# Performance work log

Hardware: AMD Instinct MI355X
Metric: run time of the kernel (lower is better)

The kernel has to match this reference:

```python
import jax, jax.numpy as jnp
import numpy as np

IN_OCT = 512
OUT_OCT = 512
BATCH = 512


def setup_inputs() -> dict:
    key = jax.random.key(0)
    kx, kw = jax.random.split(key)
    x = jax.random.normal(kx, (BATCH, IN_OCT * 8), dtype=jnp.float32)
    weight = jax.random.normal(kw, (OUT_OCT, IN_OCT, 8, 8), dtype=jnp.float32)
    bias = jnp.zeros((OUT_OCT, 8), dtype=jnp.float32)
    return {"x": x, "weight": weight, "bias": bias}


def reference(x, weight, bias):
    # x: [B, in_oct*8]; weight: [out_oct, in_oct, 8, 8]; bias: [out_oct, 8]
    B = x.shape[0]
    out_oct, in_oct = weight.shape[0], weight.shape[1]
    xo = x.reshape(B, in_oct, 8)
    # octonion_mul(x[:, j], weight[i, j]) applies the per-pair 8x8 octonion
    # left-multiplication matrix; summed over j it is one bilinear contraction.
    y = jnp.einsum("bjp,ijpk->bik", xo, weight) + bias[None, :, :]
    return y.reshape(B, out_oct * 8)
```

## Files before the change

kernel.cpp:

```cpp
#include <hip/hip_runtime.h>
#include <stdint.h>


#define M_DIM 512
#define N_DIM 4096
#define K_DIM 4096
#define KSPLIT 4
#define KC (K_DIM / KSPLIT)
#define NIT (KC / 32)
#define PART_ELEMS (M_DIM * N_DIM)

typedef __bf16 bf16x8 __attribute__((ext_vector_type(8)));
typedef float f32x4 __attribute__((ext_vector_type(4)));

__device__ inline unsigned short f2bf(float f) {
  union { float f; unsigned int u; } v;
  v.f = f;
  unsigned int u = v.u;
  unsigned int r = (u + 0x7fffu + ((u >> 16) & 1u)) >> 16;
  return (unsigned short)r;
}

__global__ __launch_bounds__(256) void prep_kernel(
    const float* __restrict__ x, const float* __restrict__ w,
    const float* __restrict__ bias, unsigned short* __restrict__ abf,
    unsigned short* __restrict__ bt, float* __restrict__ out) {
  const int bid = blockIdx.x;
  const int t = threadIdx.x;
  if (bid < 4096) {
    __shared__ __align__(16) unsigned short lT[8][512];
    const int i = bid >> 3;
    const int jg = bid & 7;
    const float4* src =
        (const float4*)(w + (size_t)i * 32768 + jg * 4096 + t * 16);
    float4 v0 = src[0], v1 = src[1], v2 = src[2], v3 = src[3];
    const int jp = (t >> 2) * 8 + (t & 3) * 2;
    const float* lo = (const float*)&v0;
    const float* hi = (const float*)&v2;
#pragma unroll
    for (int k = 0; k < 4; ++k) {
      unsigned int pk =
          (unsigned int)f2bf(lo[k]) | ((unsigned int)f2bf(hi[k]) << 16);
      *(unsigned int*)&lT[k][jp] = pk;
    }
    lo = (const float*)&v1;
    hi = (const float*)&v3;
#pragma unroll
    for (int k = 0; k < 4; ++k) {
      unsigned int pk =
          (unsigned int)f2bf(lo[k]) | ((unsigned int)f2bf(hi[k]) << 16);
      *(unsigned int*)&lT[k + 4][jp] = pk;
    }
    __syncthreads();
    const int r = t >> 5, c = t & 31;
    const uint4* s = (const uint4*)&lT[r][c * 16];
    uint4* d = (uint4*)(bt + (size_t)(i * 8 + r) * K_DIM + jg * 512 + c * 16);
    d[0] = s[0];
    d[1] = s[1];
  } else if (bid < 5120) {
    int g = (bid - 4096) * 256 + t;
    const float4* xi = (const float4*)x;
    float4 a = xi[g * 2];
    float4 b = xi[g * 2 + 1];
    __attribute__((aligned(16))) unsigned short o[8] = {
        f2bf(a.x), f2bf(a.y), f2bf(a.z), f2bf(a.w),
        f2bf(b.x), f2bf(b.y), f2bf(b.z), f2bf(b.w)};
    *(uint4*)(abf + (size_t)g * 8) = *(const uint4*)o;
  } else {
    int g = (bid - 5120) * 256 + t;
    int el = g * 4;
    int col = el & (N_DIM - 1);
    *(float4*)(out + el) = *(const float4*)(bias + col);
  }
}

__device__ inline void gld16(const void* g, void* l) {
  __builtin_amdgcn_global_load_lds(
      (const __attribute__((address_space(1))) unsigned int*)g,
      (__attribute__((address_space(3))) unsigned int*)l, 16, 0, 0);
}

__global__ __launch_bounds__(256) void gemm_kernel(
    const unsigned short* __restrict__ A, const unsigned short* __restrict__ Bt,
    float* __restrict__ out, float* __restrict__ part, int use_atomic) {
  __shared__ __align__(16) char lds[2][16 * 1024];
  const int t = threadIdx.x;
  const int n0 = blockIdx.x * 128;
  const int m0 = blockIdx.y * 128;
  const int z = blockIdx.z;
  const int kc0 = z * KC;
  const int w = t >> 6;
  const int lane = t & 63;
  const int wr = w >> 1;
  const int wc = w & 1;
  const int lrow = lane & 15;
  const int kb = lane >> 4;
  const int kslot = (kb + (lrow >> 1)) & 3;

  f32x4 acc[4][4] = {};

  const int srow = t >> 2;
  const int gslot = ((t & 3) - ((t >> 3) & 3)) & 3;
  const int scol = gslot * 8;
  const size_t aOff0 = (size_t)(m0 + srow) * K_DIM + kc0 + scol;
  const size_t aOff1 = aOff0 + (size_t)64 * K_DIM;
  const size_t bOff0 = (size_t)(n0 + srow) * K_DIM + kc0 + scol;
  const size_t bOff1 = bOff0 + (size_t)64 * K_DIM;

  auto issue = [&](int it) {
    char* buf = lds[it & 1];
    gld16(A + aOff0 + it * 32, buf + t * 16);
    gld16(A + aOff1 + it * 32, buf + 4096 + t * 16);
    gld16(Bt + bOff0 + it * 32, buf + 8192 + t * 16);
    gld16(Bt + bOff1 + it * 32, buf + 12288 + t * 16);
  };

  issue(0);
  for (int it = 0; it < NIT; ++it) {
    __syncthreads();
    if (it + 1 < NIT) issue(it + 1);
    const unsigned short* cA = (const unsigned short*)lds[it & 1];
    const unsigned short* cB = cA + 4096;

    bf16x8 af[4], bfr[4];
#pragma unroll
    for (int mt = 0; mt < 4; ++mt)
      af[mt] =
          *(const bf16x8*)(cA + (wr * 64 + mt * 16 + lrow) * 32 + kslot * 8);
#pragma unroll
    for (int nt = 0; nt < 4; ++nt)
      bfr[nt] =
          *(const bf16x8*)(cB + (wc * 64 + nt * 16 + lrow) * 32 + kslot * 8);
#pragma unroll
    for (int mt = 0; mt < 4; ++mt)
#pragma unroll
      for (int nt = 0; nt < 4; ++nt)
        acc[mt][nt] = __builtin_amdgcn_mfma_f32_16x16x32_bf16(
            af[mt], bfr[nt], acc[mt][nt], 0, 0, 0);
  }

#pragma unroll
  for (int mt = 0; mt < 4; ++mt) {
    const int gmb = m0 + wr * 64 + mt * 16 + kb * 4;
#pragma unroll
    for (int nt = 0; nt < 4; ++nt) {
      const int gn = n0 + wc * 64 + nt * 16 + lrow;
      if (use_atomic) {
#pragma unroll
        for (int r = 0; r < 4; ++r)
          atomicAdd(out + (size_t)(gmb + r) * N_DIM + gn, acc[mt][nt][r]);
      } else {
        float* p = part + (size_t)z * PART_ELEMS;
#pragma unroll
        for (int r = 0; r < 4; ++r)
          p[(size_t)(gmb + r) * N_DIM + gn] = acc[mt][nt][r];
      }
    }
  }
}

__global__ __launch_bounds__(256) void reduce_kernel(
    const float* __restrict__ part, const float* __restrict__ bias,
    float* __restrict__ out) {
  const int g = blockIdx.x * 256 + threadIdx.x;
  const float4* p = (const float4*)part;
  const float4* b4 = (const float4*)bias;
  const int Q = PART_ELEMS / 4;
  float4 s0 = p[g];
  float4 s1 = p[g + Q];
  float4 s2 = p[g + 2 * Q];
  float4 s3 = p[g + 3 * Q];
  float4 bb = b4[g & (N_DIM / 4 - 1)];
  float4 r;
  r.x = s0.x + s1.x + s2.x + s3.x + bb.x;
  r.y = s0.y + s1.y + s2.y + s3.y + bb.y;
  r.z = s0.z + s1.z + s2.z + s3.z + bb.z;
  r.w = s0.w + s1.w + s2.w + s3.w + bb.w;
  ((float4*)out)[g] = r;
}

extern "C" void kernel_launch(void* const* d_in, const int* in_sizes, int n_in,
                              void* d_out, int out_size, void* d_ws,
                              size_t ws_size, hipStream_t stream) {
  const float* x = (const float*)d_in[0];
  const float* w = (const float*)d_in[1];
  const float* bias = (const float*)d_in[2];
  float* out = (float*)d_out;

  unsigned short* abf = (unsigned short*)d_ws;
  unsigned short* bt = abf + (size_t)M_DIM * K_DIM;
  float* part = (float*)((char*)d_ws + 36u * 1024 * 1024);

  const bool have_ws = ws_size >= 68ull * 1024 * 1024;
  const int use_atomic = have_ws ? 0 : 1;

  prep_kernel<<<use_atomic ? 7168 : 5120, 256, 0, stream>>>(x, w, bias, abf,
                                                            bt, out);

  dim3 grid(N_DIM / 128, M_DIM / 128, KSPLIT);
  gemm_kernel<<<grid, 256, 0, stream>>>(abf, bt, out, part, use_atomic);

  if (!use_atomic)
    reduce_kernel<<<PART_ELEMS / 4 / 256, 256, 0, stream>>>(part, bias, out);
}
```

Before: 138.1 us.

## Fuse fp32-to-bf16 conversion and weight transpose into GEMM tile loads

```diff
diff --git a/kernel.cpp b/kernel.cpp
--- a/kernel.cpp
+++ b/kernel.cpp
@@ -13,75 +13,16 @@
 typedef __bf16 bf16x8 __attribute__((ext_vector_type(8)));
 typedef float f32x4 __attribute__((ext_vector_type(4)));
 
-__device__ inline unsigned short f2bf(float f) {
-  union { float f; unsigned int u; } v;
-  v.f = f;
-  unsigned int u = v.u;
-  unsigned int r = (u + 0x7fffu + ((u >> 16) & 1u)) >> 16;
-  return (unsigned short)r;
-}
-
-__global__ __launch_bounds__(256) void prep_kernel(
-    const float* __restrict__ x, const float* __restrict__ w,
-    const float* __restrict__ bias, unsigned short* __restrict__ abf,
-    unsigned short* __restrict__ bt, float* __restrict__ out) {
-  const int bid = blockIdx.x;
-  const int t = threadIdx.x;
-  if (bid < 4096) {
-    __shared__ __align__(16) unsigned short lT[8][512];
-    const int i = bid >> 3;
-    const int jg = bid & 7;
-    const float4* src =
-        (const float4*)(w + (size_t)i * 32768 + jg * 4096 + t * 16);
-    float4 v0 = src[0], v1 = src[1], v2 = src[2], v3 = src[3];
-    const int jp = (t >> 2) * 8 + (t & 3) * 2;
-    const float* lo = (const float*)&v0;
-    const float* hi = (const float*)&v2;
-#pragma unroll
-    for (int k = 0; k < 4; ++k) {
-      unsigned int pk =
-          (unsigned int)f2bf(lo[k]) | ((unsigned int)f2bf(hi[k]) << 16);
-      *(unsigned int*)&lT[k][jp] = pk;
-    }
-    lo = (const float*)&v1;
-    hi = (const float*)&v3;
-#pragma unroll
-    for (int k = 0; k < 4; ++k) {
-      unsigned int pk =
-          (unsigned int)f2bf(lo[k]) | ((unsigned int)f2bf(hi[k]) << 16);
-      *(unsigned int*)&lT[k + 4][jp] = pk;
-    }
-    __syncthreads();
-    const int r = t >> 5, c = t & 31;
-    const uint4* s = (const uint4*)&lT[r][c * 16];
-    uint4* d = (uint4*)(bt + (size_t)(i * 8 + r) * K_DIM + jg * 512 + c * 16);
-    d[0] = s[0];
-    d[1] = s[1];
-  } else if (bid < 5120) {
-    int g = (bid - 4096) * 256 + t;
-    const float4* xi = (const float4*)x;
-    float4 a = xi[g * 2];
-    float4 b = xi[g * 2 + 1];
-    __attribute__((aligned(16))) unsigned short o[8] = {
-        f2bf(a.x), f2bf(a.y), f2bf(a.z), f2bf(a.w),
-        f2bf(b.x), f2bf(b.y), f2bf(b.z), f2bf(b.w)};
-    *(uint4*)(abf + (size_t)g * 8) = *(const uint4*)o;
-  } else {
-    int g = (bid - 5120) * 256 + t;
-    int el = g * 4;
-    int col = el & (N_DIM - 1);
-    *(float4*)(out + el) = *(const float4*)(bias + col);
-  }
-}
-
-__device__ inline void gld16(const void* g, void* l) {
-  __builtin_amdgcn_global_load_lds(
-      (const __attribute__((address_space(1))) unsigned int*)g,
-      (__attribute__((address_space(3))) unsigned int*)l, 16, 0, 0);
+__global__ __launch_bounds__(256) void bias_init_kernel(
+    const float* __restrict__ bias, float* __restrict__ out) {
+  int g = blockIdx.x * 256 + threadIdx.x;
+  int el = g * 4;
+  int col = el & (N_DIM - 1);
+  *(float4*)(out + el) = *(const float4*)(bias + col);
 }
 
 __global__ __launch_bounds__(256) void gemm_kernel(
-    const unsigned short* __restrict__ A, const unsigned short* __restrict__ Bt,
+    const float* __restrict__ X, const float* __restrict__ W,
     float* __restrict__ out, float* __restrict__ part, int use_atomic) {
   __shared__ __align__(16) char lds[2][16 * 1024];
   const int t = threadIdx.x;
@@ -99,26 +40,86 @@
 
   f32x4 acc[4][4] = {};
 
-  const int srow = t >> 2;
-  const int gslot = ((t & 3) - ((t >> 3) & 3)) & 3;
-  const int scol = gslot * 8;
-  const size_t aOff0 = (size_t)(m0 + srow) * K_DIM + kc0 + scol;
-  const size_t aOff1 = aOff0 + (size_t)64 * K_DIM;
-  const size_t bOff0 = (size_t)(n0 + srow) * K_DIM + kc0 + scol;
-  const size_t bOff1 = bOff0 + (size_t)64 * K_DIM;
-
-  auto issue = [&](int it) {
+  const int arow = t >> 1;
+  const int ag0 = (t & 1) * 2;
+  const float* aBase = X + (size_t)(m0 + arow) * K_DIM + kc0 + ag0 * 8;
+  const int as0 = (ag0 + (arow >> 1)) & 3;
+  const int as1 = (ag0 + 1 + (arow >> 1)) & 3;
+  const int awOff0 = arow * 64 + as0 * 16;
+  const int awOff1 = arow * 64 + as1 * 16;
+
+  const int a2 = t >> 2;
+  const int jj = t & 3;
+  const int rr = a2 * 2;
+  const int nrow = n0 + rr;
+  const int iW = nrow >> 3;
+  const int kW = nrow & 7;
+  const float* wBase =
+      W + (size_t)iW * 32768 + (size_t)((kc0 >> 3) + jj) * 64 + kW;
+  const int bslot = (jj + a2) & 3;
+  const int bwOff = 8192 + rr * 64 + bslot * 16;
+
+  float4 av0, av1, av2, av3;
+  float2 bv0, bv1, bv2, bv3, bv4, bv5, bv6, bv7;
+
+  auto loadA = [&](int it) {
+    const float* p = aBase + it * 32;
+    av0 = *(const float4*)(p);
+    av1 = *(const float4*)(p + 4);
+    av2 = *(const float4*)(p + 8);
+    av3 = *(const float4*)(p + 12);
+  };
+  auto loadB = [&](int it) {
+    const float* p = wBase + it * 256;
+    bv0 = *(const float2*)(p);
+    bv1 = *(const float2*)(p + 8);
+    bv2 = *(const float2*)(p + 16);
+    bv3 = *(const float2*)(p + 24);
+    bv4 = *(const float2*)(p + 32);
+    bv5 = *(const float2*)(p + 40);
+    bv6 = *(const float2*)(p + 48);
+    bv7 = *(const float2*)(p + 56);
+  };
+  auto writeA = [&](int it) {
     char* buf = lds[it & 1];
-    gld16(A + aOff0 + it * 32, buf + t * 16);
-    gld16(A + aOff1 + it * 32, buf + 4096 + t * 16);
-    gld16(Bt + bOff0 + it * 32, buf + 8192 + t * 16);
-    gld16(Bt + bOff1 + it * 32, buf + 12288 + t * 16);
-  };
-
-  issue(0);
+    bf16x8 r0, r1;
+    r0[0] = (__bf16)av0.x; r0[1] = (__bf16)av0.y;
+    r0[2] = (__bf16)av0.z; r0[3] = (__bf16)av0.w;
+    r0[4] = (__bf16)av1.x; r0[5] = (__bf16)av1.y;
+    r0[6] = (__bf16)av1.z; r0[7] = (__bf16)av1.w;
+    r1[0] = (__bf16)av2.x; r1[1] = (__bf16)av2.y;
+    r1[2] = (__bf16)av2.z; r1[3] = (__bf16)av2.w;
+    r1[4] = (__bf16)av3.x; r1[5] = (__bf16)av3.y;
+    r1[6] = (__bf16)av3.z; r1[7] = (__bf16)av3.w;
+    *(bf16x8*)(buf + awOff0) = r0;
+    *(bf16x8*)(buf + awOff1) = r1;
+  };
+  auto writeB = [&](int it) {
+    char* buf = lds[it & 1];
+    bf16x8 r0, r1;
+    r0[0] = (__bf16)bv0.x; r1[0] = (__bf16)bv0.y;
+    r0[1] = (__bf16)bv1.x; r1[1] = (__bf16)bv1.y;
+    r0[2] = (__bf16)bv2.x; r1[2] = (__bf16)bv2.y;
+    r0[3] = (__bf16)bv3.x; r1[3] = (__bf16)bv3.y;
+    r0[4] = (__bf16)bv4.x; r1[4] = (__bf16)bv4.y;
+    r0[5] = (__bf16)bv5.x; r1[5] = (__bf16)bv5.y;
+    r0[6] = (__bf16)bv6.x; r1[6] = (__bf16)bv6.y;
+    r0[7] = (__bf16)bv7.x; r1[7] = (__bf16)bv7.y;
+    *(bf16x8*)(buf + bwOff) = r0;
+    *(bf16x8*)(buf + bwOff + 64) = r1;
+  };
+
+  loadA(0);
+  loadB(0);
+  writeA(0);
+  writeB(0);
+  __syncthreads();
+
   for (int it = 0; it < NIT; ++it) {
-    __syncthreads();
-    if (it + 1 < NIT) issue(it + 1);
+    if (it + 1 < NIT) {
+      loadA(it + 1);
+      loadB(it + 1);
+    }
     const unsigned short* cA = (const unsigned short*)lds[it & 1];
     const unsigned short* cB = cA + 4096;
 
@@ -137,6 +138,12 @@
       for (int nt = 0; nt < 4; ++nt)
         acc[mt][nt] = __builtin_amdgcn_mfma_f32_16x16x32_bf16(
             af[mt], bfr[nt], acc[mt][nt], 0, 0, 0);
+
+    if (it + 1 < NIT) {
+      writeA(it + 1);
+      writeB(it + 1);
+    }
+    __syncthreads();
   }
 
 #pragma unroll
@@ -187,18 +194,16 @@
   const float* bias = (const float*)d_in[2];
   float* out = (float*)d_out;
 
-  unsigned short* abf = (unsigned short*)d_ws;
-  unsigned short* bt = abf + (size_t)M_DIM * K_DIM;
-  float* part = (float*)((char*)d_ws + 36u * 1024 * 1024);
-
-  const bool have_ws = ws_size >= 68ull * 1024 * 1024;
-  const int use_atomic = have_ws ? 0 : 1;
-
-  prep_kernel<<<use_atomic ? 7168 : 5120, 256, 0, stream>>>(x, w, bias, abf,
-                                                            bt, out);
+  float* part = (float*)d_ws;
+
+  const bool ws_ok = ws_size >= 32ull * 1024 * 1024;
+  const int use_atomic = ws_ok ? 0 : 1;
+
+  if (use_atomic)
+    bias_init_kernel<<<PART_ELEMS / 4 / 256, 256, 0, stream>>>(bias, out);
 
   dim3 grid(N_DIM / 128, M_DIM / 128, KSPLIT);
-  gemm_kernel<<<grid, 256, 0, stream>>>(abf, bt, out, part, use_atomic);
+  gemm_kernel<<<grid, 256, 0, stream>>>(x, w, out, part, use_atomic);
 
   if (!use_atomic)
     reduce_kernel<<<PART_ELEMS / 4 / 256, 256, 0, stream>>>(part, bias, out);
```

After: 176.4 us. 1.28x slower.
